# Kernel tuning notes

Measured on AMD Instinct MI355X. Metric: run time of the kernel, lower is better.

## Reference

```python
import jax, jax.numpy as jnp
import numpy as np

B, T, IN, H, L = 8192, 200, 4, 16, 4
MLP_IN, MLP_HID, MLP_OUT = H * T, 64, IN * 7


def _lstm_layer(x, Wih, Whh, b):
    """x: [B,T,Din]; Wih: [4H,Din]; Whh: [4H,H]; b: [4H]. Returns [B,T,H].
    PyTorch gate order: i, f, g, o."""
    xg = jnp.einsum('btd,gd->btg', x, Wih) + b  # precompute input projections [B,T,4H]
    h0 = jnp.zeros((x.shape[0], H), x.dtype)
    c0 = jnp.zeros((x.shape[0], H), x.dtype)

    def step(carry, xt):
        h, c = carry
        gates = xt + h @ Whh.T  # [B,4H]
        i, f, g, o = jnp.split(gates, 4, axis=-1)
        i = jax.nn.sigmoid(i); f = jax.nn.sigmoid(f)
        g = jnp.tanh(g); o = jax.nn.sigmoid(o)
        c = f * c + i * g
        h = o * jnp.tanh(c)
        return (h, c), h

    _, hs = jax.lax.scan(step, (h0, c0), jnp.swapaxes(xg, 0, 1))  # [T,B,H]
    return jnp.swapaxes(hs, 0, 1)


def setup_inputs() -> dict:
    key = jax.random.key(0)
    ks = jax.random.split(key, 12)
    s = 1.0 / np.sqrt(H)
    u = lambda k, shp: jax.random.uniform(k, shp, jnp.float32, -s, s)
    x = jax.random.normal(ks[0], (B, T, IN), jnp.float32)
    Wih0 = u(ks[1], (4 * H, IN))            # layer 0 input weights
    Wih_rest = u(ks[2], (L - 1, 4 * H, H))  # layers 1..3
    Whh = u(ks[3], (L, 4 * H, H))
    bih = u(ks[4], (L, 4 * H))
    bhh = u(ks[5], (L, 4 * H))
    sm = 1.0 / np.sqrt(MLP_IN)
    W1 = jax.random.uniform(ks[6], (MLP_HID, MLP_IN), jnp.float32, -sm, sm)
    b1 = jax.random.uniform(ks[7], (MLP_HID,), jnp.float32, -sm, sm)
    sm2 = 1.0 / np.sqrt(MLP_HID)
    W2 = jax.random.uniform(ks[8], (MLP_OUT, MLP_HID), jnp.float32, -sm2, sm2)
    b2 = jax.random.uniform(ks[9], (MLP_OUT,), jnp.float32, -sm2, sm2)
    return {"x": x, "Wih0": Wih0, "Wih_rest": Wih_rest, "Whh": Whh,
            "bih": bih, "bhh": bhh, "W1": W1, "b1": b1, "W2": W2, "b2": b2}


def reference(x, Wih0, Wih_rest, Whh, bih, bhh, W1, b1, W2, b2):
    h = _lstm_layer(x, Wih0, Whh[0], bih[0] + bhh[0])
    for l in range(1, L):
        h = _lstm_layer(h, Wih_rest[l - 1], Whh[l], bih[l] + bhh[l])
    flat = h.reshape(-1, H * T)  # [B, 3200]
    hid = jax.nn.relu(flat @ W1.T + b1)
    return hid @ W2.T + b2  # [B, 28]
```

## Files before the change

### kernel.cpp

```cpp
#include <hip/hip_runtime.h>
#include <hip/hip_bf16.h>


typedef short  bf16x8 __attribute__((ext_vector_type(8)));
typedef float  f32x4  __attribute__((ext_vector_type(4)));

namespace {
constexpr int kT     = 200;
constexpr int kOut   = 28;
constexpr int kPairs = kT / 2;
constexpr int kSteps = kPairs + 4;
constexpr float kNLog2e  = -1.4426950408889634f;
constexpr float kN2Log2e = -2.8853900817779268f;
constexpr int kW1Elems = 64 * 3200;
}

union FragU { bf16x8 v; unsigned u[4]; };

__device__ __forceinline__ float fast_rcp(float v){ return __builtin_amdgcn_rcpf(v); }
__device__ __forceinline__ float fast_exp2(float v){ return __builtin_amdgcn_exp2f(v); }
__device__ __forceinline__ float sig_scaled(float p){ return fast_rcp(1.0f + fast_exp2(p)); }
__device__ __forceinline__ float tanh_true(float v){
  return fmaf(fast_rcp(1.0f + fast_exp2(kN2Log2e*v)), 2.0f, -1.0f);
}

__device__ __forceinline__ void split8(const float* v, FragU& hi, FragU& lo){
#pragma unroll
  for (int r=0;r<4;++r){
    unsigned ua=__float_as_uint(v[2*r]), ub=__float_as_uint(v[2*r+1]);
    hi.u[r] = (ua>>16) | (ub & 0xffff0000u);
    float af=__uint_as_float(ua & 0xffff0000u);
    float bf=__uint_as_float(ub & 0xffff0000u);
    float al=v[2*r]-af, bl=v[2*r+1]-bf;
    lo.u[r] = (__float_as_uint(al)>>16) | (__float_as_uint(bl) & 0xffff0000u);
  }
}

__global__ __launch_bounds__(256)
void presplit_w1(const float* __restrict__ W1,
                 short* __restrict__ W1h, short* __restrict__ W1l){
  int i = blockIdx.x*256 + threadIdx.x;
  if (i < kW1Elems){
    float v = W1[i];
    unsigned u = __float_as_uint(v);
    float hif = __uint_as_float(u & 0xffff0000u);
    float lo  = v - hif;
    W1h[i] = (short)(u >> 16);
    W1l[i] = (short)(__float_as_uint(lo) >> 16);
  }
}

template<bool PS>
__global__ __launch_bounds__(256)
void lstm_pipe(const float* __restrict__ x,
               const float* __restrict__ Wih0,
               const float* __restrict__ Wihr,
               const float* __restrict__ Whh,
               const float* __restrict__ bih,
               const float* __restrict__ bhh,
               const float* __restrict__ W1,
               const float* __restrict__ b1,
               const float* __restrict__ W2,
               const float* __restrict__ b2,
               const short* __restrict__ W1h,
               const short* __restrict__ W1l,
               float* __restrict__ out)
{
  __shared__ float ldsH[2][4][2][16][20];
  __shared__ float ldsR[16][68];

  const int tid  = threadIdx.x;
  const int lane = tid & 63;
  const int wv   = tid >> 6;
  const int s    = lane & 15;
  const int q    = lane >> 4;
  const int l    = wv;
  const int lm1  = (l==0) ? 0 : (l-1);
  const int sbase = blockIdx.x * 16;

  for (int i = tid; i < 2*4*2*16*20; i += 256) ((float*)ldsH)[i] = 0.f;

  FragU A[4][2];
#pragma unroll
  for (int tile=0;tile<4;++tile){
    const int grow = tile*16 + s;
    const float kE = (tile==2)? kN2Log2e : kNLog2e;
    float v[8];
    if (l==0){
#pragma unroll
      for (int e=0;e<8;++e){
        float w = 0.f;
        if (q==0 && e<4) w = Wih0[grow*4+e];
        if (q>=2)        w = Whh[grow*16 + (q&1)*8 + e];
        v[e] = w*kE;
      }
    } else {
#pragma unroll
      for (int e=0;e<8;++e){
        float w = (q<2) ? Wihr[((l-1)*64+grow)*16 + q*8 + e]
                        : Whh [(( l )*64+grow)*16 + (q&1)*8 + e];
        v[e] = w*kE;
      }
    }
    split8(v, A[tile][0], A[tile][1]);
  }

  f32x4 biasf[4];
#pragma unroll
  for (int tile=0;tile<4;++tile){
    const float kE = (tile==2)? kN2Log2e : kNLog2e;
#pragma unroll
    for (int r=0;r<4;++r){
      const int row = l*64 + tile*16 + 4*q + r;
      biasf[tile][r] = (bih[row] + bhh[row]) * kE;
    }
  }

  float cst[4] = {0.f,0.f,0.f,0.f};
  f32x4 mlpacc = (f32x4){0.f,0.f,0.f,0.f};

  const float* xp = x + (size_t)(sbase+s)*(kT*4);
  float4 xA, xB;
  if (l==0){
    xA = *(const float4*)xp;
    xB = *(const float4*)(xp+4);
  }

  const int rowW1 = wv*16 + s;
  const short* w1hp = W1h + (size_t)rowW1*3200;
  const short* w1lp = W1l + (size_t)rowW1*3200;
  const float* w1fp = W1  + (size_t)rowW1*3200;
  FragU  pWhN, pWlN, pWhC, pWlC;
  float4 pWaN, pWbN, pWaC, pWbC;

  __syncthreads();

  for (int n=0; n<kSteps; ++n){
    const int p = n & 1;
    float (*rb)[2][16][20] = ldsH[p^1];
    float (*wb)[2][16][20] = ldsH[p];

    {
      const int mp = n - 3;
      if (mp >= 0 && mp < kPairs){
        const int off = 32*mp + q*8;
        if (PS){
          pWhN.v = *(const bf16x8*)(w1hp + off);
          pWlN.v = *(const bf16x8*)(w1lp + off);
        } else {
          pWaN = *(const float4*)(w1fp + off);
          pWbN = *(const float4*)(w1fp + off + 4);
        }
      }
    }
    const int pr = n - l;
    float4 xnA, xnB;
    if (l==0 && pr+1 < kPairs){
      xnA = *(const float4*)(xp + 8*(pr+1));
      xnB = *(const float4*)(xp + 8*(pr+1) + 4);
    }

    if (pr >= 0 && pr < kPairs){
#pragma unroll
      for (int st=0; st<2; ++st){
        float bv[8];
        {
          const float* hp = (q < 2)
            ? &rb[lm1][st][s][(q&1)*8]
            : (st==0 ? &rb[l][1][s][(q&1)*8] : &wb[l][0][s][(q&1)*8]);
          const float4 h0 = *(const float4*)hp;
          const float4 h1 = *(const float4*)(hp+4);
          bv[0]=h0.x; bv[1]=h0.y; bv[2]=h0.z; bv[3]=h0.w;
          bv[4]=h1.x; bv[5]=h1.y; bv[6]=h1.z; bv[7]=h1.w;
        }
        if (l==0){
          if (q==0){
            const float4 xv = st==0 ? xA : xB;
            bv[0]=xv.x; bv[1]=xv.y; bv[2]=xv.z; bv[3]=xv.w;
            bv[4]=0.f; bv[5]=0.f; bv[6]=0.f; bv[7]=0.f;
          } else if (q==1){
#pragma unroll
            for (int e=0;e<8;++e) bv[e]=0.f;
          }
        }
        FragU Bh,Bl; split8(bv,Bh,Bl);

        float si[4], sf[4], sg[4], so[4];
#pragma unroll
        for (int tile=0;tile<4;++tile){
          f32x4 acc = biasf[tile];
          acc = __builtin_amdgcn_mfma_f32_16x16x32_bf16(A[tile][0].v,Bh.v,acc,0,0,0);
          acc = __builtin_amdgcn_mfma_f32_16x16x32_bf16(A[tile][0].v,Bl.v,acc,0,0,0);
          acc = __builtin_amdgcn_mfma_f32_16x16x32_bf16(A[tile][1].v,Bh.v,acc,0,0,0);
#pragma unroll
          for (int r=0;r<4;++r){
            const float a = sig_scaled(acc[r]);
            if      (tile==0) si[r]=a;
            else if (tile==1) sf[r]=a;
            else if (tile==2) sg[r]=fmaf(a,2.f,-1.f);
            else              so[r]=a;
          }
        }
        float hn[4];
#pragma unroll
        for (int r=0;r<4;++r){
          cst[r] = fmaf(sf[r], cst[r], si[r]*sg[r]);
          hn[r] = so[r]*tanh_true(cst[r]);
        }
        f32x4 hv = (f32x4){hn[0],hn[1],hn[2],hn[3]};
        *(f32x4*)&wb[l][st][s][4*q] = hv;
      }
    }
    if (l==0 && pr+1 < kPairs){ xA = xnA; xB = xnB; }

    {
      const int m = n - 4;
      if (m >= 0 && m < kPairs){
        float bv[8];
        {
          const float* hp3 = &rb[3][q>>1][s][(q&1)*8];
          const float4 h0 = *(const float4*)hp3;
          const float4 h1 = *(const float4*)(hp3+4);
          bv[0]=h0.x; bv[1]=h0.y; bv[2]=h0.z; bv[3]=h0.w;
          bv[4]=h1.x; bv[5]=h1.y; bv[6]=h1.z; bv[7]=h1.w;
        }
        FragU Bh,Bl; split8(bv,Bh,Bl);
        FragU Ah,Al;
        if (PS){ Ah = pWhC; Al = pWlC; }
        else {
          float v[8] = {pWaC.x,pWaC.y,pWaC.z,pWaC.w,pWbC.x,pWbC.y,pWbC.z,pWbC.w};
          split8(v,Ah,Al);
        }
        mlpacc = __builtin_amdgcn_mfma_f32_16x16x32_bf16(Ah.v,Bh.v,mlpacc,0,0,0);
        mlpacc = __builtin_amdgcn_mfma_f32_16x16x32_bf16(Ah.v,Bl.v,mlpacc,0,0,0);
        mlpacc = __builtin_amdgcn_mfma_f32_16x16x32_bf16(Al.v,Bh.v,mlpacc,0,0,0);
      }
    }
    if (PS){ pWhC = pWhN; pWlC = pWlN; }
    else   { pWaC = pWaN; pWbC = pWbN; }
    __syncthreads();
  }

  {
    f32x4 rv;
#pragma unroll
    for (int r=0;r<4;++r)
      rv[r] = fmaxf(mlpacc[r] + b1[wv*16 + 4*q + r], 0.f);
    *(f32x4*)&ldsR[s][wv*16 + 4*q] = rv;
  }
  __syncthreads();
  {
    const int o  = lane & 31;
    const int oc = (o < kOut) ? o : 0;
    float4 w2r[16];
#pragma unroll
    for (int c2=0;c2<16;++c2) w2r[c2] = *(const float4*)(W2 + oc*64 + 4*c2);
    const float bias2 = b2[oc];
#pragma unroll
    for (int mm=0;mm<2;++mm){
      const int s2 = wv*4 + 2*mm + (lane>>5);
      float a0=bias2, a1=0.f, a2=0.f, a3=0.f;
#pragma unroll
      for (int c2=0;c2<16;++c2){
        const float4 rvv = *(const float4*)&ldsR[s2][4*c2];
        a0 = fmaf(w2r[c2].x, rvv.x, a0);
        a1 = fmaf(w2r[c2].y, rvv.y, a1);
        a2 = fmaf(w2r[c2].z, rvv.z, a2);
        a3 = fmaf(w2r[c2].w, rvv.w, a3);
      }
      if (o < kOut) out[(size_t)(sbase+s2)*kOut + o] = (a0+a1)+(a2+a3);
    }
  }
}

extern "C" void kernel_launch(void* const* d_in, const int* in_sizes, int n_in,
                              void* d_out, int out_size, void* d_ws, size_t ws_size,
                              hipStream_t stream) {
  (void)in_sizes; (void)n_in; (void)out_size;
  const float* x    = (const float*)d_in[0];
  const float* Wih0 = (const float*)d_in[1];
  const float* Wihr = (const float*)d_in[2];
  const float* Whh  = (const float*)d_in[3];
  const float* bih  = (const float*)d_in[4];
  const float* bhh  = (const float*)d_in[5];
  const float* W1   = (const float*)d_in[6];
  const float* b1   = (const float*)d_in[7];
  const float* W2   = (const float*)d_in[8];
  const float* b2   = (const float*)d_in[9];
  float* out = (float*)d_out;

  const size_t splitBytes = (size_t)kW1Elems * sizeof(short) * 2;
  dim3 grid(8192/16), block(256);
  if (ws_size >= splitBytes) {
    short* W1h = (short*)d_ws;
    short* W1l = W1h + kW1Elems;
    hipLaunchKernelGGL(presplit_w1, dim3((kW1Elems+255)/256), dim3(256), 0, stream,
                       W1, W1h, W1l);
    hipLaunchKernelGGL(lstm_pipe<true>, grid, block, 0, stream,
                       x, Wih0, Wihr, Whh, bih, bhh, W1, b1, W2, b2, W1h, W1l, out);
  } else {
    hipLaunchKernelGGL(lstm_pipe<false>, grid, block, 0, stream,
                       x, Wih0, Wihr, Whh, bih, bhh, W1, b1, W2, b2,
                       (const short*)nullptr, (const short*)nullptr, out);
  }
}
```

Measured before the change: 293.4 us.

## Process four timesteps per pipeline stage and store hidden state pre-split in LDS

Each pipeline step of the wavefront-per-layer LSTM now covers four timesteps instead of two, which halves the number of block barriers (from about 104 to 54). Hidden states are written to LDS already split into bf16 hi/lo halves, so readers load MFMA fragments directly instead of re-splitting fp32 values, and LDS traffic per value shrinks. The MLP stage now consumes two K-chunks per step, with doubled W1 prefetch registers. The cost is more registers per thread and longer serial work between barriers, which may reduce overlap between layers.

```diff
diff --git a/kernel.cpp b/kernel.cpp
--- a/kernel.cpp
+++ b/kernel.cpp
@@ -4,12 +4,13 @@
 
 typedef short  bf16x8 __attribute__((ext_vector_type(8)));
 typedef float  f32x4  __attribute__((ext_vector_type(4)));
+typedef unsigned int uint2v __attribute__((ext_vector_type(2)));
 
 namespace {
-constexpr int kT     = 200;
-constexpr int kOut   = 28;
-constexpr int kPairs = kT / 2;
-constexpr int kSteps = kPairs + 4;
+constexpr int kT    = 200;
+constexpr int kOut  = 28;
+constexpr int kQ    = kT / 4;
+constexpr int kSteps = kQ + 4;
 constexpr float kNLog2e  = -1.4426950408889634f;
 constexpr float kN2Log2e = -2.8853900817779268f;
 constexpr int kW1Elems = 64 * 3200;
@@ -49,6 +50,8 @@
     W1l[i] = (short)(__float_as_uint(lo) >> 16);
   }
 }
+
+#define HIDX(pp,ll,ss,sa,jj) (((((pp)*4+(ll))*4+(ss))*16+(sa))*24+(jj))
 
 template<bool PS>
 __global__ __launch_bounds__(256)
@@ -66,7 +69,8 @@
                const short* __restrict__ W1l,
                float* __restrict__ out)
 {
-  __shared__ float ldsH[2][4][2][16][20];
+  __shared__ unsigned short Hh[2][4][4][16][24];
+  __shared__ unsigned short Hl[2][4][4][16][24];
   __shared__ float ldsR[16][68];
 
   const int tid  = threadIdx.x;
@@ -78,7 +82,10 @@
   const int lm1  = (l==0) ? 0 : (l-1);
   const int sbase = blockIdx.x * 16;
 
-  for (int i = tid; i < 2*4*2*16*20; i += 256) ((float*)ldsH)[i] = 0.f;
+  for (int i = tid; i < 2*4*4*16*24/2; i += 256){
+    ((unsigned*)Hh)[i] = 0u;
+    ((unsigned*)Hl)[i] = 0u;
+  }
 
   FragU A[4][2];
 #pragma unroll
@@ -120,70 +127,81 @@
   f32x4 mlpacc = (f32x4){0.f,0.f,0.f,0.f};
 
   const float* xp = x + (size_t)(sbase+s)*(kT*4);
-  float4 xA, xB;
+  float4 xc0,xc1,xc2,xc3;
   if (l==0){
-    xA = *(const float4*)xp;
-    xB = *(const float4*)(xp+4);
+    xc0 = *(const float4*)(xp+ 0); xc1 = *(const float4*)(xp+ 4);
+    xc2 = *(const float4*)(xp+ 8); xc3 = *(const float4*)(xp+12);
   }
 
   const int rowW1 = wv*16 + s;
   const short* w1hp = W1h + (size_t)rowW1*3200;
   const short* w1lp = W1l + (size_t)rowW1*3200;
   const float* w1fp = W1  + (size_t)rowW1*3200;
-  FragU  pWhN, pWlN, pWhC, pWlC;
-  float4 pWaN, pWbN, pWaC, pWbC;
+  FragU  pWhC0,pWlC0,pWhC1,pWlC1, pWhN0,pWlN0,pWhN1,pWlN1;
+  float4 pWaC0,pWbC0,pWaC1,pWbC1, pWaN0,pWbN0,pWaN1,pWbN1;
 
   __syncthreads();
 
+#pragma unroll 2
   for (int n=0; n<kSteps; ++n){
     const int p = n & 1;
-    float (*rb)[2][16][20] = ldsH[p^1];
-    float (*wb)[2][16][20] = ldsH[p];
 
     {
       const int mp = n - 3;
-      if (mp >= 0 && mp < kPairs){
-        const int off = 32*mp + q*8;
+      if (mp >= 0 && mp < kQ){
+        const int off = 64*mp + q*8;
         if (PS){
-          pWhN.v = *(const bf16x8*)(w1hp + off);
-          pWlN.v = *(const bf16x8*)(w1lp + off);
+          pWhN0.v = *(const bf16x8*)(w1hp + off);
+          pWlN0.v = *(const bf16x8*)(w1lp + off);
+          pWhN1.v = *(const bf16x8*)(w1hp + off + 32);
+          pWlN1.v = *(const bf16x8*)(w1lp + off + 32);
         } else {
-          pWaN = *(const float4*)(w1fp + off);
-          pWbN = *(const float4*)(w1fp + off + 4);
+          pWaN0 = *(const float4*)(w1fp + off);
+          pWbN0 = *(const float4*)(w1fp + off + 4);
+          pWaN1 = *(const float4*)(w1fp + off + 32);
+          pWbN1 = *(const float4*)(w1fp + off + 36);
         }
       }
     }
     const int pr = n - l;
-    float4 xnA, xnB;
-    if (l==0 && pr+1 < kPairs){
-      xnA = *(const float4*)(xp + 8*(pr+1));
-      xnB = *(const float4*)(xp + 8*(pr+1) + 4);
-    }
-
-    if (pr >= 0 && pr < kPairs){
-#pragma unroll
-      for (int st=0; st<2; ++st){
-        float bv[8];
-        {
-          const float* hp = (q < 2)
-            ? &rb[lm1][st][s][(q&1)*8]
-            : (st==0 ? &rb[l][1][s][(q&1)*8] : &wb[l][0][s][(q&1)*8]);
-          const float4 h0 = *(const float4*)hp;
-          const float4 h1 = *(const float4*)(hp+4);
-          bv[0]=h0.x; bv[1]=h0.y; bv[2]=h0.z; bv[3]=h0.w;
-          bv[4]=h1.x; bv[5]=h1.y; bv[6]=h1.z; bv[7]=h1.w;
-        }
+    float4 xn0,xn1,xn2,xn3;
+    if (l==0 && pr+1 < kQ){
+      const float* xq = xp + 16*(pr+1);
+      xn0 = *(const float4*)(xq+ 0); xn1 = *(const float4*)(xq+ 4);
+      xn2 = *(const float4*)(xq+ 8); xn3 = *(const float4*)(xq+12);
+    }
+
+    if (pr >= 0 && pr < kQ){
+#pragma unroll
+      for (int st=0; st<4; ++st){
+        int rp, rl, rs;
+        if (q < 2){ rp = p^1; rl = lm1; rs = st; }
+        else if (st == 0){ rp = p^1; rl = l; rs = 3; }
+        else { rp = p; rl = l; rs = st-1; }
+        const int ridx = HIDX(rp, rl, rs, s, (q&1)*8);
+        FragU Bh, Bl;
+        Bh.v = *(const bf16x8*)&((const unsigned short*)Hh)[ridx];
+        Bl.v = *(const bf16x8*)&((const unsigned short*)Hl)[ridx];
         if (l==0){
+          const float4 xv = (st==0)?xc0:(st==1)?xc1:(st==2)?xc2:xc3;
           if (q==0){
-            const float4 xv = st==0 ? xA : xB;
-            bv[0]=xv.x; bv[1]=xv.y; bv[2]=xv.z; bv[3]=xv.w;
-            bv[4]=0.f; bv[5]=0.f; bv[6]=0.f; bv[7]=0.f;
+            const unsigned u0=__float_as_uint(xv.x), u1=__float_as_uint(xv.y);
+            const unsigned u2=__float_as_uint(xv.z), u3=__float_as_uint(xv.w);
+            Bh.u[0] = (u0>>16)|(u1&0xffff0000u);
+            Bh.u[1] = (u2>>16)|(u3&0xffff0000u);
+            Bh.u[2] = 0u; Bh.u[3] = 0u;
+            const float f0 = xv.x-__uint_as_float(u0&0xffff0000u);
+            const float f1 = xv.y-__uint_as_float(u1&0xffff0000u);
+            const float f2 = xv.z-__uint_as_float(u2&0xffff0000u);
+            const float f3 = xv.w-__uint_as_float(u3&0xffff0000u);
+            Bl.u[0] = (__float_as_uint(f0)>>16)|(__float_as_uint(f1)&0xffff0000u);
+            Bl.u[1] = (__float_as_uint(f2)>>16)|(__float_as_uint(f3)&0xffff0000u);
+            Bl.u[2] = 0u; Bl.u[3] = 0u;
           } else if (q==1){
 #pragma unroll
-            for (int e=0;e<8;++e) bv[e]=0.f;
+            for (int r=0;r<4;++r){ Bh.u[r]=0u; Bl.u[r]=0u; }
           }
         }
-        FragU Bh,Bl; split8(bv,Bh,Bl);
 
         float si[4], sf[4], sg[4], so[4];
 #pragma unroll
@@ -207,37 +225,52 @@
           cst[r] = fmaf(sf[r], cst[r], si[r]*sg[r]);
           hn[r] = so[r]*tanh_true(cst[r]);
         }
-        f32x4 hv = (f32x4){hn[0],hn[1],hn[2],hn[3]};
-        *(f32x4*)&wb[l][st][s][4*q] = hv;
-      }
-    }
-    if (l==0 && pr+1 < kPairs){ xA = xnA; xB = xnB; }
+        {
+          const unsigned u0=__float_as_uint(hn[0]), u1=__float_as_uint(hn[1]);
+          const unsigned u2=__float_as_uint(hn[2]), u3=__float_as_uint(hn[3]);
+          const unsigned hi01 = (u0>>16)|(u1&0xffff0000u);
+          const unsigned hi23 = (u2>>16)|(u3&0xffff0000u);
+          const float f0 = hn[0]-__uint_as_float(u0&0xffff0000u);
+          const float f1 = hn[1]-__uint_as_float(u1&0xffff0000u);
+          const float f2 = hn[2]-__uint_as_float(u2&0xffff0000u);
+          const float f3 = hn[3]-__uint_as_float(u3&0xffff0000u);
+          const unsigned lo01 = (__float_as_uint(f0)>>16)|(__float_as_uint(f1)&0xffff0000u);
+          const unsigned lo23 = (__float_as_uint(f2)>>16)|(__float_as_uint(f3)&0xffff0000u);
+          const int widx = HIDX(p, l, st, s, 4*q);
+          *(uint2v*)&((unsigned short*)Hh)[widx] = (uint2v){hi01,hi23};
+          *(uint2v*)&((unsigned short*)Hl)[widx] = (uint2v){lo01,lo23};
+        }
+      }
+    }
+    if (l==0 && pr+1 < kQ){ xc0=xn0; xc1=xn1; xc2=xn2; xc3=xn3; }
 
     {
       const int m = n - 4;
-      if (m >= 0 && m < kPairs){
-        float bv[8];
-        {
-          const float* hp3 = &rb[3][q>>1][s][(q&1)*8];
-          const float4 h0 = *(const float4*)hp3;
-          const float4 h1 = *(const float4*)(hp3+4);
-          bv[0]=h0.x; bv[1]=h0.y; bv[2]=h0.z; bv[3]=h0.w;
-          bv[4]=h1.x; bv[5]=h1.y; bv[6]=h1.z; bv[7]=h1.w;
-        }
-        FragU Bh,Bl; split8(bv,Bh,Bl);
-        FragU Ah,Al;
-        if (PS){ Ah = pWhC; Al = pWlC; }
-        else {
-          float v[8] = {pWaC.x,pWaC.y,pWaC.z,pWaC.w,pWbC.x,pWbC.y,pWbC.z,pWbC.w};
-          split8(v,Ah,Al);
-        }
-        mlpacc = __builtin_amdgcn_mfma_f32_16x16x32_bf16(Ah.v,Bh.v,mlpacc,0,0,0);
-        mlpacc = __builtin_amdgcn_mfma_f32_16x16x32_bf16(Ah.v,Bl.v,mlpacc,0,0,0);
-        mlpacc = __builtin_amdgcn_mfma_f32_16x16x32_bf16(Al.v,Bh.v,mlpacc,0,0,0);
-      }
-    }
-    if (PS){ pWhC = pWhN; pWlC = pWlN; }
-    else   { pWaC = pWaN; pWbC = pWbN; }
+      if (m >= 0 && m < kQ){
+#pragma unroll
+        for (int pp=0; pp<2; ++pp){
+          const int bidx = HIDX(p^1, 3, 2*pp + (q>>1), s, (q&1)*8);
+          FragU Bh, Bl;
+          Bh.v = *(const bf16x8*)&((const unsigned short*)Hh)[bidx];
+          Bl.v = *(const bf16x8*)&((const unsigned short*)Hl)[bidx];
+          FragU Ah, Al;
+          if (PS){
+            Ah = pp ? pWhC1 : pWhC0;
+            Al = pp ? pWlC1 : pWlC0;
+          } else {
+            const float4 wa = pp ? pWaC1 : pWaC0;
+            const float4 wb = pp ? pWbC1 : pWbC0;
+            float v[8] = {wa.x,wa.y,wa.z,wa.w,wb.x,wb.y,wb.z,wb.w};
+            split8(v,Ah,Al);
+          }
+          mlpacc = __builtin_amdgcn_mfma_f32_16x16x32_bf16(Ah.v,Bh.v,mlpacc,0,0,0);
+          mlpacc = __builtin_amdgcn_mfma_f32_16x16x32_bf16(Ah.v,Bl.v,mlpacc,0,0,0);
+          mlpacc = __builtin_amdgcn_mfma_f32_16x16x32_bf16(Al.v,Bh.v,mlpacc,0,0,0);
+        }
+      }
+    }
+    if (PS){ pWhC0=pWhN0; pWlC0=pWlN0; pWhC1=pWhN1; pWlC1=pWlN1; }
+    else   { pWaC0=pWaN0; pWbC0=pWbN0; pWaC1=pWaN1; pWbC1=pWbN1; }
     __syncthreads();
   }
 
```

New measurement: 265.5 us. -9.5%, faster.
